# Performance work log

Hardware: AMD Instinct MI355X
Metric: run time of the kernel (lower is better)

The kernel has to match this reference:

```python
import jax, jax.numpy as jnp
import numpy as np

N_VAR = 524288   # code.n
DV = 3           # regular variable-node degree
DC = 6           # regular check-node degree
N_CHK = N_VAR * DV // DC
T = 10           # max_iterations


def setup_inputs() -> dict:
    key = jax.random.key(0)
    k1, k2, k3 = jax.random.split(key, 3)
    rng = np.random.default_rng(0)
    # Regular (3,6) Tanner graph via random socket permutation (edge list == H sparsity)
    edge_var = np.repeat(np.arange(N_VAR, dtype=np.int32), DV)
    edge_chk = rng.permutation(np.repeat(np.arange(N_CHK, dtype=np.int32), DC)).astype(np.int32)
    llr = jax.random.normal(k1, (N_VAR,), jnp.float32) * 2.0
    beta = jax.random.normal(k2, (T,), jnp.float32) * 0.1   # per-iteration dc-shared offsets
    alpha = jax.random.normal(k3, (T,), jnp.float32) * 0.1  # per-iteration dv-shared offsets
    return {"llr": llr, "beta": beta, "alpha": alpha,
            "edge_var": jnp.asarray(edge_var), "edge_chk": jnp.asarray(edge_chk),
            "n_checks": N_CHK}


def reference(llr, beta, alpha, edge_var, edge_chk, n_checks):
    E = edge_var.shape[0]
    n = llr.shape[0]
    e_idx = jnp.arange(E)

    def step(carry, ba):
        v2c, _ = carry
        b, a = ba
        mags = jnp.abs(v2c)
        sgn = jnp.sign(v2c)
        # per-check min / argmin(first) / second-min over incoming edge magnitudes
        min1 = jax.ops.segment_min(mags, edge_chk, num_segments=n_checks)
        amin = jax.ops.segment_min(jnp.where(mags == min1[edge_chk], e_idx, E),
                                   edge_chk, num_segments=n_checks)
        is_amin = e_idx == amin[edge_chk]
        min2 = jax.ops.segment_min(jnp.where(is_amin, jnp.inf, mags),
                                   edge_chk, num_segments=n_checks)
        min2 = jnp.where(jnp.isinf(min2), min1, min2)  # degree-1 checks: min2 = min1
        raw = jnp.where(is_amin, min2[edge_chk], min1[edge_chk])
        # product of signs excluding self (signs are +-1)
        sprod = jax.ops.segment_prod(sgn, edge_chk, num_segments=n_checks)
        c2v = sprod[edge_chk] * sgn * (jax.nn.relu(raw - b) - a)
        # variable node: extrinsic sum
        tot = jax.ops.segment_sum(c2v, edge_var, num_segments=n)
        v2c_new = llr[edge_var] + tot[edge_var] - c2v
        return (v2c_new, c2v), None

    v2c0 = llr[edge_var]
    (v2c_f, c2v_f), _ = jax.lax.scan(step, (v2c0, jnp.zeros_like(v2c0)), (beta, alpha))
    posterior = llr + jax.ops.segment_sum(c2v_f, edge_var, num_segments=n)
    decoded_bits = (posterior < 0).astype(jnp.int32)
    return decoded_bits, posterior
```

## Files before the change

### kernel.cpp

```cpp
#include <hip/hip_runtime.h>
#include <math.h>

#define DC_C 6
#define NRANGE 8
#define BCH 2048

__global__ void build_a(const int4* __restrict__ edge_chk4,
                        int* __restrict__ cnt,
                        int4* __restrict__ pos4,
                        int E4) {
    int t = blockIdx.x * blockDim.x + threadIdx.x;
    if (t >= E4) return;
    int4 c = edge_chk4[t];
    int j0 = atomicAdd(&cnt[c.x], 1);
    int j1 = atomicAdd(&cnt[c.y], 1);
    int j2 = atomicAdd(&cnt[c.z], 1);
    int j3 = atomicAdd(&cnt[c.w], 1);
    pos4[t] = make_int4(c.x * DC_C + j0, c.y * DC_C + j1,
                        c.z * DC_C + j2, c.w * DC_C + j3);
}

__global__ void build_b(const int4* __restrict__ pos4,
                        int* __restrict__ vmap,
                        int E) {
    int r = blockIdx.x & (NRANGE - 1);
    int chunk = blockIdx.x >> 3;
    int lo = r * (E / NRANGE);
    int hi = lo + (E / NRANGE);
    int base4 = chunk * (BCH / 4);
    int lim4 = E / 4;
#pragma unroll
    for (int rr = 0; rr < 2; ++rr) {
        int t4 = base4 + rr * 256 + threadIdx.x;
        if (t4 >= lim4) break;
        int4 p = pos4[t4];
        int e = t4 * 4;
        if (p.x >= lo && p.x < hi) vmap[p.x] = e / 3;
        if (p.y >= lo && p.y < hi) vmap[p.y] = (e + 1) / 3;
        if (p.z >= lo && p.z < hi) vmap[p.z] = (e + 2) / 3;
        if (p.w >= lo && p.w < hi) vmap[p.w] = (e + 3) / 3;
    }
}

__global__ void check_kernel(const float* __restrict__ p,
                             const int* __restrict__ vmap,
                             float* __restrict__ c2v_s,
                             const float* __restrict__ beta,
                             const float* __restrict__ alpha,
                             int t, int n_chk) {
    int c = blockIdx.x * blockDim.x + threadIdx.x;
    if (c >= n_chk) return;
    int base = c * DC_C;
    int2 w01 = *(const int2*)(vmap + base);
    int2 w23 = *(const int2*)(vmap + base + 2);
    int2 w45 = *(const int2*)(vmap + base + 4);
    float2 o01 = *(const float2*)(c2v_s + base);
    float2 o23 = *(const float2*)(c2v_s + base + 2);
    float2 o45 = *(const float2*)(c2v_s + base + 4);
    int   w[DC_C]   = {w01.x, w01.y, w23.x, w23.y, w45.x, w45.y};
    float old_[DC_C] = {o01.x, o01.y, o23.x, o23.y, o45.x, o45.y};
    float pv[DC_C];
#pragma unroll
    for (int j = 0; j < DC_C; ++j) pv[j] = p[w[j]];
    float b = beta[t];
    float a = alpha[t];
    float sg[DC_C], mg[DC_C];
    float sprod = 1.0f;
    float m1 = INFINITY, m2 = INFINITY;
#pragma unroll
    for (int j = 0; j < DC_C; ++j) {
        float x = pv[j] - old_[j];
        float s = (x > 0.0f) ? 1.0f : ((x < 0.0f) ? -1.0f : 0.0f);
        float m = fabsf(x);
        sg[j] = s;
        mg[j] = m;
        sprod *= s;
        if (m < m1) { m2 = m1; m1 = m; }
        else if (m < m2) { m2 = m; }
    }
    float o[DC_C];
#pragma unroll
    for (int j = 0; j < DC_C; ++j) {
        float raw = (mg[j] == m1) ? m2 : m1;
        float val = fmaxf(raw - b, 0.0f) - a;
        o[j] = sprod * sg[j] * val;
    }
    *(float2*)(c2v_s + base)     = make_float2(o[0], o[1]);
    *(float2*)(c2v_s + base + 2) = make_float2(o[2], o[3]);
    *(float2*)(c2v_s + base + 4) = make_float2(o[4], o[5]);
}

__global__ void var_kernel(const float* __restrict__ c2v_s,
                           const int* __restrict__ pos,
                           const float* __restrict__ llr,
                           float* __restrict__ p,
                           int n) {
    int v = blockIdx.x * blockDim.x + threadIdx.x;
    if (v >= n) return;
    int p0 = pos[v * 3 + 0];
    int p1 = pos[v * 3 + 1];
    int p2 = pos[v * 3 + 2];
    float c0 = c2v_s[p0];
    float c1 = c2v_s[p1];
    float c2 = c2v_s[p2];
    p[v] = llr[v] + ((c0 + c1) + c2);
}

__global__ void final_kernel(const float* __restrict__ c2v_s,
                             const int* __restrict__ pos,
                             const float* __restrict__ llr,
                             float* __restrict__ out,
                             int n) {
    int v = blockIdx.x * blockDim.x + threadIdx.x;
    if (v >= n) return;
    int p0 = pos[v * 3 + 0];
    int p1 = pos[v * 3 + 1];
    int p2 = pos[v * 3 + 2];
    float c0 = c2v_s[p0];
    float c1 = c2v_s[p1];
    float c2 = c2v_s[p2];
    float post = llr[v] + ((c0 + c1) + c2);
    out[v] = (post < 0.0f) ? 1.0f : 0.0f;
    out[n + v] = post;
}

extern "C" void kernel_launch(void* const* d_in, const int* in_sizes, int n_in,
                              void* d_out, int out_size, void* d_ws, size_t ws_size,
                              hipStream_t stream) {
    const float* llr      = (const float*)d_in[0];
    const float* beta     = (const float*)d_in[1];
    const float* alpha    = (const float*)d_in[2];
    const int*   edge_chk = (const int*)d_in[4];

    const int n  = in_sizes[0];
    const int T  = in_sizes[1];
    const int E  = in_sizes[3];
    const int n_chk = E / DC_C;

    char* ws = (char*)d_ws;
    int*   cnt   = (int*)ws;
    int*   pos   = (int*)(ws + (size_t)n_chk * 4);
    int*   vmap  = pos + E;
    float* c2v_s = (float*)(vmap + E);
    float* p     = c2v_s + E;

    hipMemsetAsync(cnt, 0, (size_t)n_chk * 4, stream);
    hipMemsetAsync(c2v_s, 0, (size_t)E * 4, stream);
    {
        int E4 = E / 4;
        build_a<<<(E4 + 255) / 256, 256, 0, stream>>>((const int4*)edge_chk,
                                                      cnt, (int4*)pos, E4);
    }
    {
        int chunks = (E + BCH - 1) / BCH;
        build_b<<<chunks * NRANGE, 256, 0, stream>>>((const int4*)pos, vmap, E);
    }
    for (int t = 0; t < T; ++t) {
        const float* src = (t == 0) ? llr : p;
        check_kernel<<<(n_chk + 255) / 256, 256, 0, stream>>>(
            src, vmap, c2v_s, beta, alpha, t, n_chk);
        if (t + 1 < T) {
            var_kernel<<<(n + 255) / 256, 256, 0, stream>>>(c2v_s, pos, llr, p, n);
        } else {
            final_kernel<<<(n + 255) / 256, 256, 0, stream>>>(c2v_s, pos, llr,
                                                              (float*)d_out, n);
        }
    }
}
```

Baseline: 411.5 us.

## Store compressed per-check min-sum records instead of per-edge c2v messages

```diff
diff --git a/kernel.cpp b/kernel.cpp
--- a/kernel.cpp
+++ b/kernel.cpp
@@ -3,122 +3,158 @@
 
 #define DC_C 6
 #define NRANGE 8
-#define BCH 2048
-
-__global__ void build_a(const int4* __restrict__ edge_chk4,
+#define VCH 2048
+
+
+__global__ void build_a(const int* __restrict__ edge_chk,
                         int* __restrict__ cnt,
-                        int4* __restrict__ pos4,
-                        int E4) {
-    int t = blockIdx.x * blockDim.x + threadIdx.x;
-    if (t >= E4) return;
-    int4 c = edge_chk4[t];
-    int j0 = atomicAdd(&cnt[c.x], 1);
-    int j1 = atomicAdd(&cnt[c.y], 1);
-    int j2 = atomicAdd(&cnt[c.z], 1);
-    int j3 = atomicAdd(&cnt[c.w], 1);
-    pos4[t] = make_int4(c.x * DC_C + j0, c.y * DC_C + j1,
-                        c.z * DC_C + j2, c.w * DC_C + j3);
-}
-
-__global__ void build_b(const int4* __restrict__ pos4,
+                        unsigned long long* __restrict__ pos64,
+                        int n) {
+    int v = blockIdx.x * blockDim.x + threadIdx.x;
+    if (v >= n) return;
+    int c0 = edge_chk[v * 3 + 0];
+    int c1 = edge_chk[v * 3 + 1];
+    int c2 = edge_chk[v * 3 + 2];
+    int j0 = atomicAdd(&cnt[c0], 1);
+    int j1 = atomicAdd(&cnt[c1], 1);
+    int j2 = atomicAdd(&cnt[c2], 1);
+    unsigned long long s0 = (unsigned long long)(c0 * DC_C + j0);
+    unsigned long long s1 = (unsigned long long)(c1 * DC_C + j1);
+    unsigned long long s2 = (unsigned long long)(c2 * DC_C + j2);
+    pos64[v] = s0 | (s1 << 21) | (s2 << 42);
+}
+
+__global__ void build_b(const unsigned long long* __restrict__ pos64,
                         int* __restrict__ vmap,
-                        int E) {
+                        int n, int E) {
     int r = blockIdx.x & (NRANGE - 1);
     int chunk = blockIdx.x >> 3;
     int lo = r * (E / NRANGE);
     int hi = lo + (E / NRANGE);
-    int base4 = chunk * (BCH / 4);
-    int lim4 = E / 4;
-#pragma unroll
-    for (int rr = 0; rr < 2; ++rr) {
-        int t4 = base4 + rr * 256 + threadIdx.x;
-        if (t4 >= lim4) break;
-        int4 p = pos4[t4];
-        int e = t4 * 4;
-        if (p.x >= lo && p.x < hi) vmap[p.x] = e / 3;
-        if (p.y >= lo && p.y < hi) vmap[p.y] = (e + 1) / 3;
-        if (p.z >= lo && p.z < hi) vmap[p.z] = (e + 2) / 3;
-        if (p.w >= lo && p.w < hi) vmap[p.w] = (e + 3) / 3;
+    int base = chunk * VCH;
+#pragma unroll
+    for (int rr = 0; rr < VCH / 256; ++rr) {
+        int v = base + rr * 256 + threadIdx.x;
+        if (v >= n) break;
+        unsigned long long pk = pos64[v];
+        int s0 = (int)(pk & 0x1FFFFF);
+        int s1 = (int)((pk >> 21) & 0x1FFFFF);
+        int s2 = (int)((pk >> 42) & 0x1FFFFF);
+        if (s0 >= lo && s0 < hi) vmap[s0] = v;
+        if (s1 >= lo && s1 < hi) vmap[s1] = v;
+        if (s2 >= lo && s2 < hi) vmap[s2] = v;
     }
 }
 
 __global__ void check_kernel(const float* __restrict__ p,
                              const int* __restrict__ vmap,
-                             float* __restrict__ c2v_s,
+                             float4* __restrict__ recs,
                              const float* __restrict__ beta,
                              const float* __restrict__ alpha,
-                             int t, int n_chk) {
+                             int t, int n_chk, int first) {
     int c = blockIdx.x * blockDim.x + threadIdx.x;
     if (c >= n_chk) return;
     int base = c * DC_C;
     int2 w01 = *(const int2*)(vmap + base);
     int2 w23 = *(const int2*)(vmap + base + 2);
     int2 w45 = *(const int2*)(vmap + base + 4);
-    float2 o01 = *(const float2*)(c2v_s + base);
-    float2 o23 = *(const float2*)(c2v_s + base + 2);
-    float2 o45 = *(const float2*)(c2v_s + base + 4);
-    int   w[DC_C]   = {w01.x, w01.y, w23.x, w23.y, w45.x, w45.y};
-    float old_[DC_C] = {o01.x, o01.y, o23.x, o23.y, o45.x, o45.y};
+    int w[DC_C] = {w01.x, w01.y, w23.x, w23.y, w45.x, w45.y};
     float pv[DC_C];
 #pragma unroll
     for (int j = 0; j < DC_C; ++j) pv[j] = p[w[j]];
+
+    float old_[DC_C];
+    if (first) {
+#pragma unroll
+        for (int j = 0; j < DC_C; ++j) old_[j] = 0.0f;
+    } else {
+        float4 rec = recs[c];
+        unsigned int mk = __float_as_uint(rec.z);
+        unsigned int am = mk & 0x3F;
+        unsigned int ng = (mk >> 8) & 0x3F;
+        unsigned int zr = (mk >> 16) & 0x3F;
+#pragma unroll
+        for (int j = 0; j < DC_C; ++j) {
+            float val = ((am >> j) & 1) ? rec.x : rec.y;
+            float s = ((zr >> j) & 1) ? 0.0f : (((ng >> j) & 1) ? -1.0f : 1.0f);
+            old_[j] = s * val;
+        }
+    }
+
     float b = beta[t];
     float a = alpha[t];
-    float sg[DC_C], mg[DC_C];
     float sprod = 1.0f;
     float m1 = INFINITY, m2 = INFINITY;
+    float mg[DC_C];
+    unsigned int ng = 0, zr = 0;
 #pragma unroll
     for (int j = 0; j < DC_C; ++j) {
         float x = pv[j] - old_[j];
-        float s = (x > 0.0f) ? 1.0f : ((x < 0.0f) ? -1.0f : 0.0f);
         float m = fabsf(x);
-        sg[j] = s;
         mg[j] = m;
-        sprod *= s;
+        if (x < 0.0f) { ng |= (1u << j); sprod = -sprod; }
+        else if (x == 0.0f) { zr |= (1u << j); sprod = 0.0f; }
         if (m < m1) { m2 = m1; m1 = m; }
         else if (m < m2) { m2 = m; }
     }
-    float o[DC_C];
-#pragma unroll
-    for (int j = 0; j < DC_C; ++j) {
-        float raw = (mg[j] == m1) ? m2 : m1;
-        float val = fmaxf(raw - b, 0.0f) - a;
-        o[j] = sprod * sg[j] * val;
-    }
-    *(float2*)(c2v_s + base)     = make_float2(o[0], o[1]);
-    *(float2*)(c2v_s + base + 2) = make_float2(o[2], o[3]);
-    *(float2*)(c2v_s + base + 4) = make_float2(o[4], o[5]);
-}
-
-__global__ void var_kernel(const float* __restrict__ c2v_s,
-                           const int* __restrict__ pos,
+    unsigned int am = 0;
+#pragma unroll
+    for (int j = 0; j < DC_C; ++j) am |= (mg[j] == m1) ? (1u << j) : 0u;
+    float A = fmaxf(m2 - b, 0.0f) - a;
+    float B = fmaxf(m1 - b, 0.0f) - a;
+    float4 out;
+    out.x = sprod * A;
+    out.y = sprod * B;
+    out.z = __uint_as_float(am | (ng << 8) | (zr << 16));
+    out.w = 0.0f;
+    recs[c] = out;
+}
+
+__device__ __forceinline__ float c2v_from_rec(float4 rec, int j) {
+    unsigned int mk = __float_as_uint(rec.z);
+    float val = ((mk >> j) & 1) ? rec.x : rec.y;
+    float s = ((mk >> (16 + j)) & 1) ? 0.0f
+            : (((mk >> (8 + j)) & 1) ? -1.0f : 1.0f);
+    return s * val;
+}
+
+__global__ void var_kernel(const float4* __restrict__ recs,
+                           const unsigned long long* __restrict__ pos64,
                            const float* __restrict__ llr,
                            float* __restrict__ p,
                            int n) {
     int v = blockIdx.x * blockDim.x + threadIdx.x;
     if (v >= n) return;
-    int p0 = pos[v * 3 + 0];
-    int p1 = pos[v * 3 + 1];
-    int p2 = pos[v * 3 + 2];
-    float c0 = c2v_s[p0];
-    float c1 = c2v_s[p1];
-    float c2 = c2v_s[p2];
+    unsigned long long pk = pos64[v];
+    int s0 = (int)(pk & 0x1FFFFF);
+    int s1 = (int)((pk >> 21) & 0x1FFFFF);
+    int s2 = (int)((pk >> 42) & 0x1FFFFF);
+    float4 r0 = recs[s0 / DC_C];
+    float4 r1 = recs[s1 / DC_C];
+    float4 r2 = recs[s2 / DC_C];
+    float c0 = c2v_from_rec(r0, s0 % DC_C);
+    float c1 = c2v_from_rec(r1, s1 % DC_C);
+    float c2 = c2v_from_rec(r2, s2 % DC_C);
     p[v] = llr[v] + ((c0 + c1) + c2);
 }
 
-__global__ void final_kernel(const float* __restrict__ c2v_s,
-                             const int* __restrict__ pos,
+__global__ void final_kernel(const float4* __restrict__ recs,
+                             const unsigned long long* __restrict__ pos64,
                              const float* __restrict__ llr,
                              float* __restrict__ out,
                              int n) {
     int v = blockIdx.x * blockDim.x + threadIdx.x;
     if (v >= n) return;
-    int p0 = pos[v * 3 + 0];
-    int p1 = pos[v * 3 + 1];
-    int p2 = pos[v * 3 + 2];
-    float c0 = c2v_s[p0];
-    float c1 = c2v_s[p1];
-    float c2 = c2v_s[p2];
+    unsigned long long pk = pos64[v];
+    int s0 = (int)(pk & 0x1FFFFF);
+    int s1 = (int)((pk >> 21) & 0x1FFFFF);
+    int s2 = (int)((pk >> 42) & 0x1FFFFF);
+    float4 r0 = recs[s0 / DC_C];
+    float4 r1 = recs[s1 / DC_C];
+    float4 r2 = recs[s2 / DC_C];
+    float c0 = c2v_from_rec(r0, s0 % DC_C);
+    float c1 = c2v_from_rec(r1, s1 % DC_C);
+    float c2 = c2v_from_rec(r2, s2 % DC_C);
     float post = llr[v] + ((c0 + c1) + c2);
     out[v] = (post < 0.0f) ? 1.0f : 0.0f;
     out[n + v] = post;
@@ -138,31 +174,26 @@
     const int n_chk = E / DC_C;
 
     char* ws = (char*)d_ws;
-    int*   cnt   = (int*)ws;
-    int*   pos   = (int*)(ws + (size_t)n_chk * 4);
-    int*   vmap  = pos + E;
-    float* c2v_s = (float*)(vmap + E);
-    float* p     = c2v_s + E;
+    int*                 cnt   = (int*)ws;
+    unsigned long long*  pos64 = (unsigned long long*)(ws + (1u << 20));
+    int*                 vmap  = (int*)(ws + (5u << 20));
+    float4*              recs  = (float4*)(ws + (11u << 20));
+    float*               p     = (float*)(ws + (15u << 20));
 
     hipMemsetAsync(cnt, 0, (size_t)n_chk * 4, stream);
-    hipMemsetAsync(c2v_s, 0, (size_t)E * 4, stream);
+    build_a<<<(n + 255) / 256, 256, 0, stream>>>(edge_chk, cnt, pos64, n);
     {
-        int E4 = E / 4;
-        build_a<<<(E4 + 255) / 256, 256, 0, stream>>>((const int4*)edge_chk,
-                                                      cnt, (int4*)pos, E4);
-    }
-    {
-        int chunks = (E + BCH - 1) / BCH;
-        build_b<<<chunks * NRANGE, 256, 0, stream>>>((const int4*)pos, vmap, E);
+        int chunks = (n + VCH - 1) / VCH;
+        build_b<<<chunks * NRANGE, 256, 0, stream>>>(pos64, vmap, n, E);
     }
     for (int t = 0; t < T; ++t) {
         const float* src = (t == 0) ? llr : p;
         check_kernel<<<(n_chk + 255) / 256, 256, 0, stream>>>(
-            src, vmap, c2v_s, beta, alpha, t, n_chk);
+            src, vmap, recs, beta, alpha, t, n_chk, (t == 0) ? 1 : 0);
         if (t + 1 < T) {
-            var_kernel<<<(n + 255) / 256, 256, 0, stream>>>(c2v_s, pos, llr, p, n);
+            var_kernel<<<(n + 255) / 256, 256, 0, stream>>>(recs, pos64, llr, p, n);
         } else {
-            final_kernel<<<(n + 255) / 256, 256, 0, stream>>>(c2v_s, pos, llr,
+            final_kernel<<<(n + 255) / 256, 256, 0, stream>>>(recs, pos64, llr,
                                                               (float*)d_out, n);
         }
     }
```

Measured after the change: 373.7 us. 1.1x faster.
